# Optimization experiments

Hardware: AMD Instinct MI355X
Metric: run time of the kernel (lower is better)

Reference implementation:

```python
import jax, jax.numpy as jnp
import numpy as np

EPS = 1e-5
K = 64  # nsample

def lrelu(x):
    return jnp.where(x > 0, x, 0.1 * x)

def bn_eval(x, g, b):
    # eval-mode BatchNorm1d with running_mean=0, running_var=1
    return x * (g / jnp.sqrt(1.0 + EPS))[None, :, None] + b[None, :, None]


def setup_inputs() -> dict:
    key = jax.random.key(0)
    ks = jax.random.split(key, 32)
    B, N1, N2, C, LC = 128, 21, 4096, 256, 256
    H = LC // 2  # 128
    s = 0.05
    inp = {
        'xyz1': jax.random.normal(ks[0], (B, 3, N1), jnp.float32),
        'xyz2': jax.random.normal(ks[1], (B, 3, N2), jnp.float32),
        'points1': jax.random.normal(ks[2], (B, LC, N1), jnp.float32),
        'points2': jax.random.normal(ks[3], (B, C, N2), jnp.float32),
        'bf_w1': jax.random.normal(ks[4], (H, LC), jnp.float32) * s,
        'bf_bias1': jax.random.normal(ks[5], (H, N1), jnp.float32) * s,
        'bf_g1': jnp.ones((H,), jnp.float32),
        'bf_be1': jnp.zeros((H,), jnp.float32),
        'bf_w2': jax.random.normal(ks[6], (H, H), jnp.float32) * s,
        'bf_bias2': jax.random.normal(ks[7], (H, N1), jnp.float32) * s,
        'bf_g2': jnp.ones((H,), jnp.float32),
        'bf_be2': jnp.zeros((H,), jnp.float32),
        'bf_w3': jax.random.normal(ks[8], (H, H), jnp.float32) * s,
        'bf_bias3': jax.random.normal(ks[9], (H, N1), jnp.float32) * s,
        'bf_g3': jnp.ones((H,), jnp.float32),
        'bf_be3': jnp.zeros((H,), jnp.float32),
        # mlp (Conv2d 1x1 with bias): in = 256 + 128 + 3 = 387
        'mlp_w1': jax.random.normal(ks[10], (256, C + H + 3), jnp.float32) * s,
        'mlp_b1': jnp.zeros((256,), jnp.float32),
        'mlp_w2': jax.random.normal(ks[11], (256, 256), jnp.float32) * s,
        'mlp_b2': jnp.zeros((256,), jnp.float32),
        'mlp_w3': jax.random.normal(ks[12], (256, 256), jnp.float32) * s,
        'mlp_b3': jnp.zeros((256,), jnp.float32),
        # mlp2 (Conv1d 1x1, no bias)
        'mlp2_w1': jax.random.normal(ks[13], (256, 256), jnp.float32) * s,
        'mlp2_w2': jax.random.normal(ks[14], (256, 256), jnp.float32) * s,
        'reg_w': jax.random.normal(ks[15], (3, 256), jnp.float32) * s,
        'reg_b': jnp.zeros((3,), jnp.float32),
    }
    return inp


def reference(xyz1, xyz2, points1, points2,
              bf_w1, bf_bias1, bf_g1, bf_be1,
              bf_w2, bf_bias2, bf_g2, bf_be2,
              bf_w3, bf_bias3, bf_g3, bf_be3,
              mlp_w1, mlp_b1, mlp_w2, mlp_b2, mlp_w3, mlp_b3,
              mlp2_w1, mlp2_w2, reg_w, reg_b):
    # --- biasfold on joint features [B, LC, N1] ---
    x = points1
    for w, bb, g, be in ((bf_w1, bf_bias1, bf_g1, bf_be1),
                         (bf_w2, bf_bias2, bf_g2, bf_be2),
                         (bf_w3, bf_bias3, bf_g3, bf_be3)):
        x = lrelu(bn_eval(jnp.einsum('oc,bcn->bon', w, x) + bb[None], g, be))
    p1 = x.transpose(0, 2, 1)            # [B, N1, 128]

    x1 = xyz1.transpose(0, 2, 1)         # [B, N1, 3]
    x2 = xyz2.transpose(0, 2, 1)         # [B, N2, 3]
    p2 = points2.transpose(0, 2, 1)      # [B, N2, C]

    # --- squared pairwise distance + kNN ---
    sqr = (jnp.sum(x1 ** 2, -1)[:, :, None]
           + jnp.sum(x2 ** 2, -1)[:, None, :]
           - 2.0 * jnp.einsum('bnc,bmc->bnm', x1, x2))   # [B, N1, N2]
    _, knn_idx = jax.lax.top_k(-sqr, K)                  # [B, N1, K]

    gather = jax.vmap(lambda pts, idx: pts[idx])
    neighbor_xyz = gather(x2, knn_idx)                   # [B, N1, K, 3]
    direction_xyz = neighbor_xyz - x1[:, :, None, :]
    g2 = gather(p2, knn_idx)                             # [B, N1, K, C]
    g1 = jnp.broadcast_to(p1[:, :, None, :], knn_idx.shape + (p1.shape[-1],))
    feat = jnp.concatenate([g1, g2, direction_xyz], -1)  # [B, N1, K, 387]

    # --- shared 1x1 conv MLP (channels-last einsum) ---
    for w, b in ((mlp_w1, mlp_b1), (mlp_w2, mlp_b2), (mlp_w3, mlp_b3)):
        feat = lrelu(jnp.einsum('oc,bnkc->bnko', w, feat) + b)

    pooled = jnp.max(feat, axis=2)                       # [B, N1, 256] max over K

    for w in (mlp2_w1, mlp2_w2):
        pooled = lrelu(jnp.einsum('oc,bnc->bno', w, pooled))

    out = jnp.einsum('oc,bnc->bno', reg_w, pooled) + reg_b  # [B, N1, 3]
    return out.transpose(0, 2, 1)                           # [B, 3, N1]
```

## Files before the change

kernel.cpp:

```cpp
#include <hip/hip_runtime.h>
#include <float.h>

#define BB 128
#define N1 21
#define N2 4096
#define CC 256
#define LCH 256
#define HH 128
#define KNN 64
#define KP 268

typedef _Float16 f16;
typedef f16 f16x4 __attribute__((ext_vector_type(4)));
typedef f16 f16x8 __attribute__((ext_vector_type(8)));
typedef float f32x4 __attribute__((ext_vector_type(4)));

static const size_t OFF_A1  = 0;
static const size_t OFF_KNN = OFF_A1 + (size_t)BB * N1 * 256;
static const size_t OFF_W4T = OFF_KNN + (size_t)BB * N1 * KNN;
static const size_t OFF_W5T = OFF_W4T + 65536;
static const size_t OFF_P1H = OFF_W5T + 65536;
static const size_t OFF_P2H = OFF_P1H + 32768;
static const size_t OFF_P3H = OFF_P2H + 32768;
static const size_t OFF_P2T = OFF_P3H + 32768;

__device__ __forceinline__ float lrelu(float x) { return x > 0.f ? x : 0.1f * x; }
__device__ __forceinline__ unsigned short bits16(f16 h) { unsigned short r; __builtin_memcpy(&r, &h, 2); return r; }


__device__ __forceinline__ void pack_one(int e, const float* __restrict__ w, int stride, int koff,
                                         f16* __restrict__ hi) {
  int j = e & 7, lane = (e >> 3) & 63, ntg = (e >> 9) & 15, ks = e >> 13;
  int n = ntg * 16 + (lane & 15);
  int k = ks * 32 + 4 * (lane >> 4) + (j & 3) + 16 * (j >> 2);
  hi[e] = (f16)w[(size_t)n * stride + koff + k];
}

__global__ __launch_bounds__(256) void k_pack(
    const float* __restrict__ w1, const float* __restrict__ w2,
    const float* __restrict__ w3, const float* __restrict__ w4,
    const float* __restrict__ w5, float* __restrict__ ws) {
  int t = blockIdx.x * 256 + threadIdx.x;
  if (t < 131072) {
    int m = t >> 16, v = t & 65535;
    int c = v >> 8, o = v & 255;
    const float* src = m ? w5 : w4;
    float* dst = ws + (m ? OFF_W5T : OFF_W4T);
    dst[v] = src[o * 256 + c];
    return;
  }
  int u = t - 131072;
  if (u < 65536) { pack_one(u, w1, 387, 128, (f16*)(ws + OFF_P1H)); return; }
  u -= 65536;
  if (u < 65536) { pack_one(u, w2, 256, 0, (f16*)(ws + OFF_P2H)); return; }
  u -= 65536;
  if (u < 65536) { pack_one(u, w3, 256, 0, (f16*)(ws + OFF_P3H)); return; }
}

__global__ __launch_bounds__(256) void k_t2(
    const float* __restrict__ points2, unsigned short* __restrict__ p2t) {
  __shared__ unsigned short tile[64][66];
  int bid = blockIdx.x;
  int b = bid >> 8;
  int rem = bid & 255;
  int n0 = (rem >> 2) << 6;
  int c0 = (rem & 3) << 6;
  int t = threadIdx.x;
  int tl = t & 63, tg = t >> 6;

  const float* src = points2 + ((size_t)b * CC) * N2;
  float v[16];
  #pragma unroll
  for (int i = 0; i < 16; i++)
    v[i] = src[(size_t)(c0 + tg * 16 + i) * N2 + n0 + tl];
  #pragma unroll
  for (int i = 0; i < 16; i++)
    tile[tg * 16 + i][tl] = bits16((f16)v[i]);
  __syncthreads();
  unsigned short* dst = p2t + ((size_t)b * N2) * CC;
  unsigned short o[16];
  #pragma unroll
  for (int i = 0; i < 16; i++) o[i] = tile[tl][tg * 16 + i];
  #pragma unroll
  for (int i = 0; i < 16; i++)
    dst[(size_t)(n0 + tg * 16 + i) * CC + c0 + tl] = o[i];
}

__global__ __launch_bounds__(128) void k_biasfold(
    const float* __restrict__ points1,
    const float* __restrict__ w1, const float* __restrict__ bb1,
    const float* __restrict__ g1, const float* __restrict__ be1,
    const float* __restrict__ w2, const float* __restrict__ bb2,
    const float* __restrict__ g2, const float* __restrict__ be2,
    const float* __restrict__ w3, const float* __restrict__ bb3,
    const float* __restrict__ g3, const float* __restrict__ be3,
    const float* __restrict__ w1mlp,
    float* __restrict__ A1out) {
  int blk = blockIdx.x;
  int b = blk / N1, n = blk % N1;
  int t = threadIdx.x;
  __shared__ float x0[LCH], x1s[HH], x2s[HH], x3s[HH];
  const float bnS = 1.0f / sqrtf(1.0f + 1e-5f);

  x0[t]       = points1[((size_t)b * LCH + t) * N1 + n];
  x0[t + 128] = points1[((size_t)b * LCH + t + 128) * N1 + n];
  __syncthreads();
  {
    float acc = 0.f;
    const float* wr = w1 + (size_t)t * LCH;
    #pragma unroll 4
    for (int c = 0; c < LCH; c++) acc += wr[c] * x0[c];
    acc += bb1[t * N1 + n];
    acc = acc * (g1[t] * bnS) + be1[t];
    x1s[t] = lrelu(acc);
  }
  __syncthreads();
  {
    float acc = 0.f;
    const float* wr = w2 + (size_t)t * HH;
    #pragma unroll 4
    for (int c = 0; c < HH; c++) acc += wr[c] * x1s[c];
    acc += bb2[t * N1 + n];
    acc = acc * (g2[t] * bnS) + be2[t];
    x2s[t] = lrelu(acc);
  }
  __syncthreads();
  {
    float acc = 0.f;
    const float* wr = w3 + (size_t)t * HH;
    #pragma unroll 4
    for (int c = 0; c < HH; c++) acc += wr[c] * x2s[c];
    acc += bb3[t * N1 + n];
    acc = acc * (g3[t] * bnS) + be3[t];
    x3s[t] = lrelu(acc);
  }
  __syncthreads();
  #pragma unroll
  for (int rep = 0; rep < 2; rep++) {
    int o = t + rep * 128;
    const float* wr = w1mlp + (size_t)o * 387;
    float acc = 0.f;
    #pragma unroll 4
    for (int c = 0; c < HH; c++) acc += wr[c] * x3s[c];
    A1out[(size_t)blk * 256 + o] = acc;
  }
}

__global__ __launch_bounds__(256) void k_knn(
    const float* __restrict__ xyz1, const float* __restrict__ xyz2,
    int* __restrict__ knn) {
  int blk = blockIdx.x;
  int b = blk / N1, n = blk % N1;
  int t = threadIdx.x;
  __shared__ float wvv[4];
  __shared__ int wii[4];

  float ax = xyz1[((size_t)b * 3 + 0) * N1 + n];
  float ay = xyz1[((size_t)b * 3 + 1) * N1 + n];
  float az = xyz1[((size_t)b * 3 + 2) * N1 + n];
  float xx1 = ax * ax + ay * ay + az * az;
  const float* X = xyz2 + (size_t)b * 3 * N2;

  float dl[16];
  #pragma unroll
  for (int i = 0; i < 16; i++) {
    int j = t + i * 256;
    float px = X[j], py = X[N2 + j], pz = X[2 * N2 + j];
    float xx2 = px * px + py * py + pz * pz;
    float dot = ax * px + ay * py + az * pz;
    dl[i] = (xx1 + xx2) - 2.0f * dot;
  }

  int* out = knn + (size_t)blk * KNN;
  for (int it = 0; it < KNN; it++) {
    float best = dl[0]; int bs = 0;
    #pragma unroll
    for (int i = 1; i < 16; i++)
      if (dl[i] < best) { best = dl[i]; bs = i; }
    int bi = t + bs * 256;
    #pragma unroll
    for (int off = 32; off; off >>= 1) {
      float ov = __shfl_down(best, off);
      int oi = __shfl_down(bi, off);
      if (ov < best || (ov == best && oi < bi)) { best = ov; bi = oi; }
    }
    int w = t >> 6;
    if ((t & 63) == 0) { wvv[w] = best; wii[w] = bi; }
    __syncthreads();
    float bv = wvv[0]; int bj = wii[0];
    #pragma unroll
    for (int p = 1; p < 4; p++)
      if (wvv[p] < bv || (wvv[p] == bv && wii[p] < bj)) { bv = wvv[p]; bj = wii[p]; }
    if (t == 0) out[it] = bj;
    if ((bj & 255) == t) {
      int slot = bj >> 8;
      #pragma unroll
      for (int i = 0; i < 16; i++)
        if (i == slot) dl[i] = FLT_MAX;
    }
    __syncthreads();
  }
}

__device__ __forceinline__ void run_layer64(
    const f16* __restrict__ BH, const f16* Xh,
    int w, int lane, int r16, int g, f32x4 acc[4][4]) {
  #pragma unroll 1
  for (int ks = 0; ks < 8; ks++) {
    f16x8 Bh[4];
    #pragma unroll
    for (int nt = 0; nt < 4; nt++) {
      size_t fi = ((size_t)((ks * 16 + w * 4 + nt) * 64 + lane)) * 8;
      Bh[nt] = *(const f16x8*)(BH + fi);
    }
    int k0 = ks * 32 + 4 * g;
    f16x8 Ah[4];
    #pragma unroll
    for (int mt = 0; mt < 4; mt++) {
      int base = (mt * 16 + r16) * KP + k0;
      f16x4 h0 = *(const f16x4*)(Xh + base);
      f16x4 h1 = *(const f16x4*)(Xh + base + 16);
      Ah[mt] = __builtin_shufflevector(h0, h1, 0, 1, 2, 3, 4, 5, 6, 7);
    }
    #pragma unroll
    for (int mt = 0; mt < 4; mt++)
      #pragma unroll
      for (int nt = 0; nt < 4; nt++)
        acc[mt][nt] = __builtin_amdgcn_mfma_f32_16x16x32_f16(Ah[mt], Bh[nt], acc[mt][nt], 0, 0, 0);
  }
}

__device__ __forceinline__ void writeback_act64(
    f32x4 acc[4][4], const float* __restrict__ bias,
    f16* Xh, int w, int r16, int g) {
  #pragma unroll
  for (int nt = 0; nt < 4; nt++) {
    int nl = w * 64 + nt * 16 + r16;
    float bv = bias[nl];
    #pragma unroll
    for (int mt = 0; mt < 4; mt++)
      #pragma unroll
      for (int j = 0; j < 4; j++) {
        int m = mt * 16 + 4 * g + j;
        Xh[m * KP + nl] = (f16)lrelu(acc[mt][nt][j] + bv);
      }
  }
}

template <int TRANS>
__global__ __launch_bounds__(256) void k_fused9(
    const float* __restrict__ xyz1, const float* __restrict__ xyz2,
    const float* __restrict__ points2, const unsigned short* __restrict__ p2t,
    const float* __restrict__ A1ws, const int* __restrict__ knn,
    const float* __restrict__ w1mlp,
    const f16* __restrict__ P1H, const f16* __restrict__ P2H,
    const f16* __restrict__ P3H,
    const float* __restrict__ b1, const float* __restrict__ b2,
    const float* __restrict__ b3,
    const float* __restrict__ W4T, const float* __restrict__ W5T,
    const float* __restrict__ regw, const float* __restrict__ regb,
    float* __restrict__ out) {
  int bid = blockIdx.x;
  int xcd = bid & 7, slot = bid >> 3;
  int b = xcd * 16 + slot / 21;
  int n1 = slot % 21;
  int row = b * N1 + n1;

  int t = threadIdx.x;
  int lane = t & 63, w = t >> 6;
  int r16 = lane & 15, g = lane >> 4;

  __shared__ __align__(16) f16 Xhi[64 * KP];
  __shared__ float dirs[64][3];
  __shared__ int idxs[KNN];
  __shared__ float x1p[3];

  if (t < KNN) idxs[t] = knn[(size_t)row * KNN + t];
  if (t < 3) x1p[t] = xyz1[((size_t)b * 3 + t) * N1 + n1];
  __syncthreads();

  float a1v[4], wd0[4], wd1[4], wd2[4];
  #pragma unroll
  for (int nt = 0; nt < 4; nt++) {
    int n = w * 64 + nt * 16 + r16;
    a1v[nt] = A1ws[(size_t)row * 256 + n];
    wd0[nt] = w1mlp[(size_t)n * 387 + 384];
    wd1[nt] = w1mlp[(size_t)n * 387 + 385];
    wd2[nt] = w1mlp[(size_t)n * 387 + 386];
  }

  const float* x2b = xyz2 + (size_t)b * 3 * N2;
  if (t < 64) {
    int id = idxs[t];
    #pragma unroll
    for (int d = 0; d < 3; d++)
      dirs[t][d] = x2b[(size_t)d * N2 + id] - x1p[d];
  }
  if (TRANS) {
    int r = t >> 2, qq = t & 3;
    int id = idxs[r];
    const uint4* src = (const uint4*)(p2t + ((size_t)b * N2 + id) * CC + qq * 64);
    #pragma unroll
    for (int i = 0; i < 8; i++) {
      uint4 v = src[i];
      f16x8 val;
      __builtin_memcpy(&val, &v, 16);
      f16x4 lo4 = __builtin_shufflevector(val, val, 0, 1, 2, 3);
      f16x4 hi4 = __builtin_shufflevector(val, val, 4, 5, 6, 7);
      int cpos = r * KP + qq * 64 + i * 8;
      *(f16x4*)(Xhi + cpos) = lo4;
      *(f16x4*)(Xhi + cpos + 4) = hi4;
    }
  } else {
    int r = t >> 2, qq = t & 3;
    int id = idxs[r];
    const float* src = points2 + (size_t)b * CC * N2 + id;
    #pragma unroll 4
    for (int i = 0; i < 64; i++) {
      int c = qq * 64 + i;
      Xhi[r * KP + c] = (f16)src[(size_t)c * N2];
    }
  }
  __syncthreads();

  f32x4 acc[4][4];
  #pragma unroll
  for (int mt = 0; mt < 4; mt++)
    #pragma unroll
    for (int nt = 0; nt < 4; nt++)
      #pragma unroll
      for (int j = 0; j < 4; j++) {
        int m = mt * 16 + 4 * g + j;
        acc[mt][nt][j] = a1v[nt] + wd0[nt] * dirs[m][0]
                                 + wd1[nt] * dirs[m][1]
                                 + wd2[nt] * dirs[m][2];
      }
  run_layer64(P1H, Xhi, w, lane, r16, g, acc);
  __syncthreads();
  writeback_act64(acc, b1, Xhi, w, r16, g);
  __syncthreads();

  #pragma unroll
  for (int mt = 0; mt < 4; mt++)
    #pragma unroll
    for (int nt = 0; nt < 4; nt++) acc[mt][nt] = (f32x4){0.f, 0.f, 0.f, 0.f};
  run_layer64(P2H, Xhi, w, lane, r16, g, acc);
  __syncthreads();
  writeback_act64(acc, b2, Xhi, w, r16, g);
  __syncthreads();

  #pragma unroll
  for (int mt = 0; mt < 4; mt++)
    #pragma unroll
    for (int nt = 0; nt < 4; nt++) acc[mt][nt] = (f32x4){0.f, 0.f, 0.f, 0.f};
  run_layer64(P3H, Xhi, w, lane, r16, g, acc);

  float poolm[4];
  #pragma unroll
  for (int nt = 0; nt < 4; nt++) {
    float m = -FLT_MAX;
    #pragma unroll
    for (int mt = 0; mt < 4; mt++)
      #pragma unroll
      for (int j = 0; j < 4; j++) m = fmaxf(m, acc[mt][nt][j]);
    m = fmaxf(m, __shfl_xor(m, 16));
    m = fmaxf(m, __shfl_xor(m, 32));
    poolm[nt] = m;
  }
  __syncthreads();

  float* fb = (float*)Xhi;
  if (g == 0) {
    #pragma unroll
    for (int nt = 0; nt < 4; nt++) {
      int n = w * 64 + nt * 16 + r16;
      fb[n] = lrelu(poolm[nt] + b3[n]);
    }
  }
  __syncthreads();
  {
    float a = 0.f;
    #pragma unroll 4
    for (int c = 0; c < 256; c++) a += W4T[(size_t)c * 256 + t] * fb[c];
    fb[256 + t] = lrelu(a);
  }
  __syncthreads();
  {
    float a = 0.f;
    #pragma unroll 4
    for (int c = 0; c < 256; c++) a += W5T[(size_t)c * 256 + t] * fb[256 + c];
    fb[512 + t] = lrelu(a);
  }
  __syncthreads();
  if (t < 192) {
    int o = t >> 6;
    float a = 0.f;
    #pragma unroll
    for (int i = 0; i < 4; i++) {
      int c = (t & 63) + 64 * i;
      a += regw[o * 256 + c] * fb[512 + c];
    }
    #pragma unroll
    for (int off = 32; off; off >>= 1) a += __shfl_xor(a, off);
    if ((t & 63) == 0) out[((size_t)b * 3 + o) * N1 + n1] = a + regb[o];
  }
}

extern "C" void kernel_launch(void* const* d_in, const int* in_sizes, int n_in,
                              void* d_out, int out_size, void* d_ws, size_t ws_size,
                              hipStream_t stream) {
  const float* xyz1    = (const float*)d_in[0];
  const float* xyz2    = (const float*)d_in[1];
  const float* points1 = (const float*)d_in[2];
  const float* points2 = (const float*)d_in[3];
  const float* bf_w1 = (const float*)d_in[4],  *bf_b1 = (const float*)d_in[5];
  const float* bf_g1 = (const float*)d_in[6],  *bf_e1 = (const float*)d_in[7];
  const float* bf_w2 = (const float*)d_in[8],  *bf_b2 = (const float*)d_in[9];
  const float* bf_g2 = (const float*)d_in[10], *bf_e2 = (const float*)d_in[11];
  const float* bf_w3 = (const float*)d_in[12], *bf_b3 = (const float*)d_in[13];
  const float* bf_g3 = (const float*)d_in[14], *bf_e3 = (const float*)d_in[15];
  const float* mlp_w1 = (const float*)d_in[16], *mlp_b1 = (const float*)d_in[17];
  const float* mlp_w2 = (const float*)d_in[18], *mlp_b2 = (const float*)d_in[19];
  const float* mlp_w3 = (const float*)d_in[20], *mlp_b3 = (const float*)d_in[21];
  const float* mlp2_w1 = (const float*)d_in[22], *mlp2_w2 = (const float*)d_in[23];
  const float* reg_w = (const float*)d_in[24], *reg_b = (const float*)d_in[25];

  float* ws  = (float*)d_ws;
  float* A1  = ws + OFF_A1;
  int*   knn = (int*)(ws + OFF_KNN);
  unsigned short* p2t = (unsigned short*)(ws + OFF_P2T);

  float* out = (float*)d_out;
  int rows = BB * N1;

  size_t need_bytes = OFF_P2T * sizeof(float) + (size_t)BB * N2 * CC * sizeof(unsigned short);
  bool use_trans = (ws_size >= need_bytes);

  k_pack<<<1280, 256, 0, stream>>>(mlp_w1, mlp_w2, mlp_w3, mlp2_w1, mlp2_w2, ws);
  if (use_trans)
    k_t2<<<BB * 256, 256, 0, stream>>>(points2, p2t);
  k_biasfold<<<rows, 128, 0, stream>>>(points1,
      bf_w1, bf_b1, bf_g1, bf_e1,
      bf_w2, bf_b2, bf_g2, bf_e2,
      bf_w3, bf_b3, bf_g3, bf_e3, mlp_w1, A1);
  k_knn<<<rows, 256, 0, stream>>>(xyz1, xyz2, knn);
  if (use_trans)
    k_fused9<1><<<rows, 256, 0, stream>>>(xyz1, xyz2, points2, p2t, A1, knn, mlp_w1,
        (const f16*)(ws + OFF_P1H), (const f16*)(ws + OFF_P2H), (const f16*)(ws + OFF_P3H),
        mlp_b1, mlp_b2, mlp_b3,
        ws + OFF_W4T, ws + OFF_W5T, reg_w, reg_b, out);
  else
    k_fused9<0><<<rows, 256, 0, stream>>>(xyz1, xyz2, points2, p2t, A1, knn, mlp_w1,
        (const f16*)(ws + OFF_P1H), (const f16*)(ws + OFF_P2H), (const f16*)(ws + OFF_P3H),
        mlp_b1, mlp_b2, mlp_b3,
        ws + OFF_W4T, ws + OFF_W5T, reg_w, reg_b, out);
}
```

Before: 689.6 us.

## Mark kNN-selected points and transpose only used points2 columns

kNN now records which xyz2 points were selected in a per-batch byte mask (zeroed by a new kernel). The transpose kernel runs after kNN and writes only rows for selected points, which cuts the fp16 transposed write traffic. It still reads all of points2. kNN also drops one barrier per iteration by double-buffering the cross-wave reduction slots, and the fused kernel reorders its prologue loads so the gather is issued first. Costs are an extra launch, a serial dependency of the transpose on kNN, and mask loads.

```diff
diff --git a/kernel.cpp b/kernel.cpp
--- a/kernel.cpp
+++ b/kernel.cpp
@@ -15,14 +15,15 @@
 typedef f16 f16x8 __attribute__((ext_vector_type(8)));
 typedef float f32x4 __attribute__((ext_vector_type(4)));
 
-static const size_t OFF_A1  = 0;
-static const size_t OFF_KNN = OFF_A1 + (size_t)BB * N1 * 256;
-static const size_t OFF_W4T = OFF_KNN + (size_t)BB * N1 * KNN;
-static const size_t OFF_W5T = OFF_W4T + 65536;
-static const size_t OFF_P1H = OFF_W5T + 65536;
-static const size_t OFF_P2H = OFF_P1H + 32768;
-static const size_t OFF_P3H = OFF_P2H + 32768;
-static const size_t OFF_P2T = OFF_P3H + 32768;
+static const size_t OFF_A1   = 0;
+static const size_t OFF_KNN  = OFF_A1 + (size_t)BB * N1 * 256;
+static const size_t OFF_W4T  = OFF_KNN + (size_t)BB * N1 * KNN;
+static const size_t OFF_W5T  = OFF_W4T + 65536;
+static const size_t OFF_P1H  = OFF_W5T + 65536;
+static const size_t OFF_P2H  = OFF_P1H + 32768;
+static const size_t OFF_P3H  = OFF_P2H + 32768;
+static const size_t OFF_USED = OFF_P3H + 32768;
+static const size_t OFF_P2T  = OFF_USED + 131072;
 
 __device__ __forceinline__ float lrelu(float x) { return x > 0.f ? x : 0.1f * x; }
 __device__ __forceinline__ unsigned short bits16(f16 h) { unsigned short r; __builtin_memcpy(&r, &h, 2); return r; }
@@ -57,33 +58,8 @@
   if (u < 65536) { pack_one(u, w3, 256, 0, (f16*)(ws + OFF_P3H)); return; }
 }
 
-__global__ __launch_bounds__(256) void k_t2(
-    const float* __restrict__ points2, unsigned short* __restrict__ p2t) {
-  __shared__ unsigned short tile[64][66];
-  int bid = blockIdx.x;
-  int b = bid >> 8;
-  int rem = bid & 255;
-  int n0 = (rem >> 2) << 6;
-  int c0 = (rem & 3) << 6;
-  int t = threadIdx.x;
-  int tl = t & 63, tg = t >> 6;
-
-  const float* src = points2 + ((size_t)b * CC) * N2;
-  float v[16];
-  #pragma unroll
-  for (int i = 0; i < 16; i++)
-    v[i] = src[(size_t)(c0 + tg * 16 + i) * N2 + n0 + tl];
-  #pragma unroll
-  for (int i = 0; i < 16; i++)
-    tile[tg * 16 + i][tl] = bits16((f16)v[i]);
-  __syncthreads();
-  unsigned short* dst = p2t + ((size_t)b * N2) * CC;
-  unsigned short o[16];
-  #pragma unroll
-  for (int i = 0; i < 16; i++) o[i] = tile[tl][tg * 16 + i];
-  #pragma unroll
-  for (int i = 0; i < 16; i++)
-    dst[(size_t)(n0 + tg * 16 + i) * CC + c0 + tl] = o[i];
+__global__ __launch_bounds__(256) void k_zero(unsigned int* __restrict__ used32) {
+  used32[blockIdx.x * 256 + threadIdx.x] = 0;
 }
 
 __global__ __launch_bounds__(128) void k_biasfold(
@@ -148,12 +124,12 @@
 
 __global__ __launch_bounds__(256) void k_knn(
     const float* __restrict__ xyz1, const float* __restrict__ xyz2,
-    int* __restrict__ knn) {
+    int* __restrict__ knn, unsigned char* __restrict__ used) {
   int blk = blockIdx.x;
   int b = blk / N1, n = blk % N1;
   int t = threadIdx.x;
-  __shared__ float wvv[4];
-  __shared__ int wii[4];
+  __shared__ float wvv[2][4];
+  __shared__ int wii[2][4];
 
   float ax = xyz1[((size_t)b * 3 + 0) * N1 + n];
   float ay = xyz1[((size_t)b * 3 + 1) * N1 + n];
@@ -172,6 +148,7 @@
   }
 
   int* out = knn + (size_t)blk * KNN;
+  unsigned char* ub = used + (size_t)b * N2;
   for (int it = 0; it < KNN; it++) {
     float best = dl[0]; int bs = 0;
     #pragma unroll
@@ -185,21 +162,56 @@
       if (ov < best || (ov == best && oi < bi)) { best = ov; bi = oi; }
     }
     int w = t >> 6;
-    if ((t & 63) == 0) { wvv[w] = best; wii[w] = bi; }
+    int sl = it & 1;
+    if ((t & 63) == 0) { wvv[sl][w] = best; wii[sl][w] = bi; }
     __syncthreads();
-    float bv = wvv[0]; int bj = wii[0];
+    float bv = wvv[sl][0]; int bj = wii[sl][0];
     #pragma unroll
     for (int p = 1; p < 4; p++)
-      if (wvv[p] < bv || (wvv[p] == bv && wii[p] < bj)) { bv = wvv[p]; bj = wii[p]; }
-    if (t == 0) out[it] = bj;
+      if (wvv[sl][p] < bv || (wvv[sl][p] == bv && wii[sl][p] < bj)) { bv = wvv[sl][p]; bj = wii[sl][p]; }
+    if (t == 0) { out[it] = bj; ub[bj] = 1; }
     if ((bj & 255) == t) {
       int slot = bj >> 8;
       #pragma unroll
       for (int i = 0; i < 16; i++)
         if (i == slot) dl[i] = FLT_MAX;
     }
-    __syncthreads();
-  }
+  }
+}
+
+__global__ __launch_bounds__(256) void k_t2(
+    const float* __restrict__ points2, unsigned short* __restrict__ p2t,
+    const unsigned char* __restrict__ used) {
+  __shared__ unsigned short tile[64][66];
+  int bid = blockIdx.x;
+  int b = bid >> 8;
+  int rem = bid & 255;
+  int n0 = (rem >> 2) << 6;
+  int c0 = (rem & 3) << 6;
+  int t = threadIdx.x;
+  int tl = t & 63, tg = t >> 6;
+
+  const float* src = points2 + ((size_t)b * CC) * N2;
+  float v[16];
+  #pragma unroll
+  for (int i = 0; i < 16; i++)
+    v[i] = src[(size_t)(c0 + tg * 16 + i) * N2 + n0 + tl];
+  #pragma unroll
+  for (int i = 0; i < 16; i++)
+    tile[tg * 16 + i][tl] = bits16((f16)v[i]);
+
+  uint4 ubv = *(const uint4*)(used + (size_t)b * N2 + n0 + tg * 16);
+  const unsigned char* ubb = (const unsigned char*)&ubv;
+
+  __syncthreads();
+  unsigned short* dst = p2t + ((size_t)b * N2) * CC;
+  unsigned short o[16];
+  #pragma unroll
+  for (int i = 0; i < 16; i++) o[i] = tile[tl][tg * 16 + i];
+  #pragma unroll
+  for (int i = 0; i < 16; i++)
+    if (ubb[i])
+      dst[(size_t)(n0 + tg * 16 + i) * CC + c0 + tl] = o[i];
 }
 
 __device__ __forceinline__ void run_layer64(
@@ -279,23 +291,6 @@
   if (t < 3) x1p[t] = xyz1[((size_t)b * 3 + t) * N1 + n1];
   __syncthreads();
 
-  float a1v[4], wd0[4], wd1[4], wd2[4];
-  #pragma unroll
-  for (int nt = 0; nt < 4; nt++) {
-    int n = w * 64 + nt * 16 + r16;
-    a1v[nt] = A1ws[(size_t)row * 256 + n];
-    wd0[nt] = w1mlp[(size_t)n * 387 + 384];
-    wd1[nt] = w1mlp[(size_t)n * 387 + 385];
-    wd2[nt] = w1mlp[(size_t)n * 387 + 386];
-  }
-
-  const float* x2b = xyz2 + (size_t)b * 3 * N2;
-  if (t < 64) {
-    int id = idxs[t];
-    #pragma unroll
-    for (int d = 0; d < 3; d++)
-      dirs[t][d] = x2b[(size_t)d * N2 + id] - x1p[d];
-  }
   if (TRANS) {
     int r = t >> 2, qq = t & 3;
     int id = idxs[r];
@@ -320,6 +315,23 @@
       int c = qq * 64 + i;
       Xhi[r * KP + c] = (f16)src[(size_t)c * N2];
     }
+  }
+  const float* x2b = xyz2 + (size_t)b * 3 * N2;
+  if (t < 64) {
+    int id = idxs[t];
+    #pragma unroll
+    for (int d = 0; d < 3; d++)
+      dirs[t][d] = x2b[(size_t)d * N2 + id] - x1p[d];
+  }
+
+  float a1v[4], wd0[4], wd1[4], wd2[4];
+  #pragma unroll
+  for (int nt = 0; nt < 4; nt++) {
+    int n = w * 64 + nt * 16 + r16;
+    a1v[nt] = A1ws[(size_t)row * 256 + n];
+    wd0[nt] = w1mlp[(size_t)n * 387 + 384];
+    wd1[nt] = w1mlp[(size_t)n * 387 + 385];
+    wd2[nt] = w1mlp[(size_t)n * 387 + 386];
   }
   __syncthreads();
 
@@ -428,6 +440,7 @@
   float* ws  = (float*)d_ws;
   float* A1  = ws + OFF_A1;
   int*   knn = (int*)(ws + OFF_KNN);
+  unsigned char* used = (unsigned char*)(ws + OFF_USED);
   unsigned short* p2t = (unsigned short*)(ws + OFF_P2T);
 
   float* out = (float*)d_out;
@@ -437,21 +450,22 @@
   bool use_trans = (ws_size >= need_bytes);
 
   k_pack<<<1280, 256, 0, stream>>>(mlp_w1, mlp_w2, mlp_w3, mlp2_w1, mlp2_w2, ws);
-  if (use_trans)
-    k_t2<<<BB * 256, 256, 0, stream>>>(points2, p2t);
   k_biasfold<<<rows, 128, 0, stream>>>(points1,
       bf_w1, bf_b1, bf_g1, bf_e1,
       bf_w2, bf_b2, bf_g2, bf_e2,
       bf_w3, bf_b3, bf_g3, bf_e3, mlp_w1, A1);
-  k_knn<<<rows, 256, 0, stream>>>(xyz1, xyz2, knn);
-  if (use_trans)
+  k_zero<<<512, 256, 0, stream>>>((unsigned int*)used);
+  k_knn<<<rows, 256, 0, stream>>>(xyz1, xyz2, knn, used);
+  if (use_trans) {
+    k_t2<<<BB * 256, 256, 0, stream>>>(points2, p2t, used);
     k_fused9<1><<<rows, 256, 0, stream>>>(xyz1, xyz2, points2, p2t, A1, knn, mlp_w1,
         (const f16*)(ws + OFF_P1H), (const f16*)(ws + OFF_P2H), (const f16*)(ws + OFF_P3H),
         mlp_b1, mlp_b2, mlp_b3,
         ws + OFF_W4T, ws + OFF_W5T, reg_w, reg_b, out);
-  else
+  } else {
     k_fused9<0><<<rows, 256, 0, stream>>>(xyz1, xyz2, points2, p2t, A1, knn, mlp_w1,
         (const f16*)(ws + OFF_P1H), (const f16*)(ws + OFF_P2H), (const f16*)(ws + OFF_P3H),
         mlp_b1, mlp_b2, mlp_b3,
         ws + OFF_W4T, ws + OFF_W5T, reg_w, reg_b, out);
-}
+  }
+}
```

After: 657.4 us (median of 2 runs). 4.7% less time.
